# Performance work log

Measured on AMD Instinct MI355X. Metric: run time of the kernel, lower is better.

Reference implementation:

```python
import jax, jax.numpy as jnp
import numpy as np

# ViT-Small config
L, D, H, HD = 12, 384, 6, 64
P, IMG, NCLS = 16, 224, 1000
NPATCH = (IMG // P) ** 2  # 196
GAMMA, MIN_TOKENS, EPS = 0.5, 16, 1e-6
SCALE = HD ** -0.5


def _ln(x, w, b, eps=1e-6):
    mu = jnp.mean(x, axis=-1, keepdims=True)
    var = jnp.var(x, axis=-1, keepdims=True)
    return (x - mu) * jax.lax.rsqrt(var + eps) * w + b


def _qkv_split(xn, w, b):
    # xn: [B, Nt, D] -> q,k,v each [B, H, Nt, HD]
    B, Nt, _ = xn.shape
    qkv = (xn @ w.T + b).reshape(B, Nt, 3, H, HD).transpose(2, 0, 3, 1, 4)
    return qkv[0], qkv[1], qkv[2]


def _vit_forward(x, patch_w, patch_b, cls_token, pos_embed,
                 ln1_w, ln1_b, qkv_w, qkv_b, proj_w, proj_b,
                 ln2_w, ln2_b, fc1_w, fc1_b, fc2_w, fc2_b,
                 norm_w, norm_b, head_w, head_b, keep_schedule=None):
    B = x.shape[0]
    # patch embed: conv stride 16 -> [B, D, 14, 14] -> [B, 196, D]
    xp = jax.lax.conv_general_dilated(x, patch_w, (P, P), 'VALID',
                                      dimension_numbers=('NCHW', 'OIHW', 'NCHW'))
    xp = xp.reshape(B, D, NPATCH).transpose(0, 2, 1) + patch_b
    cls = jnp.broadcast_to(cls_token, (B, 1, D))
    xt = jnp.concatenate([cls, xp], axis=1) + pos_embed  # [B, 197, D]

    N = NPATCH
    prev_mass = jnp.asarray(1.0, jnp.float32)
    schedule = []
    for l in range(L):
        if keep_schedule is not None:
            keep_idx = keep_schedule[l]
        elif N > MIN_TOKENS:
            # CLS-only attention importance scoring (cheap pass)
            xn = _ln(xt, ln1_w[l], ln1_b[l])
            q, k, v = _qkv_split(xn, qkv_w[l], qkv_b[l])
            a_cls = jax.nn.softmax(jnp.einsum('bhqd,bhkd->bhqk', q[:, :, :1], k) * SCALE, axis=-1)[:, :, 0, :]  # [B,H,Nt]
            vnorm = jnp.linalg.norm(v, axis=-1)  # [B,H,Nt]
            imp = (a_cls * vnorm).mean(axis=1)   # [B,Nt]
            imp_p = imp[:, 1:]                   # patch importance
            mass = jnp.mean(imp_p.sum(-1) / (imp.sum(-1) + EPS))
            keep_ratio = float(jnp.clip(GAMMA * mass / (prev_mass + EPS), 0.0, 1.0))
            N_next = max(MIN_TOKENS, int(N * keep_ratio))
            if N_next < N:
                scores = imp_p.mean(0)  # shared keep set across batch (index_select semantics)
                top = jax.lax.top_k(scores, N_next)[1]
                keep_idx = jnp.concatenate([jnp.zeros((1,), jnp.int32),
                                            jnp.sort(top).astype(jnp.int32) + 1])
            else:
                keep_idx = None
            prev_mass = mass
        else:
            keep_idx = None
        schedule.append(keep_idx)
        if keep_idx is not None:
            xt = jnp.take(xt, keep_idx, axis=1)
            N = int(keep_idx.shape[0]) - 1

        # full transformer block on surviving tokens
        Nt = xt.shape[1]
        xn = _ln(xt, ln1_w[l], ln1_b[l])
        q, k, v = _qkv_split(xn, qkv_w[l], qkv_b[l])
        a = jax.nn.softmax(jnp.einsum('bhqd,bhkd->bhqk', q, k) * SCALE, axis=-1)
        o = jnp.einsum('bhqk,bhkd->bhqd', a, v).transpose(0, 2, 1, 3).reshape(B, Nt, D)
        xt = xt + o @ proj_w[l].T + proj_b[l]
        h = _ln(xt, ln2_w[l], ln2_b[l])
        h = jax.nn.gelu(h @ fc1_w[l].T + fc1_b[l], approximate=False)
        xt = xt + h @ fc2_w[l].T + fc2_b[l]

    xt = _ln(xt, norm_w, norm_b)
    logits = xt[:, 0] @ head_w.T + head_b
    return logits, schedule


def setup_inputs() -> dict:
    key = jax.random.key(0)
    ks = jax.random.split(key, 10)
    rn = lambda k, s, sc=0.02: jax.random.normal(k, s, jnp.float32) * sc
    return {
        'x': jax.random.normal(ks[0], (64, 3, IMG, IMG), jnp.float32),
        'patch_w': rn(ks[1], (D, 3, P, P)),
        'patch_b': jnp.zeros((D,), jnp.float32),
        'cls_token': rn(ks[2], (1, 1, D)),
        'pos_embed': rn(ks[3], (1, NPATCH + 1, D)),
        'ln1_w': jnp.ones((L, D), jnp.float32), 'ln1_b': jnp.zeros((L, D), jnp.float32),
        'qkv_w': rn(ks[4], (L, 3 * D, D)), 'qkv_b': jnp.zeros((L, 3 * D), jnp.float32),
        'proj_w': rn(ks[5], (L, D, D)), 'proj_b': jnp.zeros((L, D), jnp.float32),
        'ln2_w': jnp.ones((L, D), jnp.float32), 'ln2_b': jnp.zeros((L, D), jnp.float32),
        'fc1_w': rn(ks[6], (L, 4 * D, D)), 'fc1_b': jnp.zeros((L, 4 * D), jnp.float32),
        'fc2_w': rn(ks[7], (L, D, 4 * D)), 'fc2_b': jnp.zeros((L, D), jnp.float32),
        'norm_w': jnp.ones((D,), jnp.float32), 'norm_b': jnp.zeros((D,), jnp.float32),
        'head_w': rn(ks[8], (NCLS, D)), 'head_b': jnp.zeros((NCLS,), jnp.float32),
    }


def reference(x, patch_w, patch_b, cls_token, pos_embed, ln1_w, ln1_b, qkv_w, qkv_b,
              proj_w, proj_b, ln2_w, ln2_b, fc1_w, fc1_b, fc2_w, fc2_b,
              norm_w, norm_b, head_w, head_b):
    logits, _ = _vit_forward(x, patch_w, patch_b, cls_token, pos_embed, ln1_w, ln1_b,
                             qkv_w, qkv_b, proj_w, proj_b, ln2_w, ln2_b,
                             fc1_w, fc1_b, fc2_w, fc2_b, norm_w, norm_b, head_w, head_b)
    return logits
```

## Files before the change

kernel.cpp:

```cpp
#include <hip/hip_runtime.h>
#include <hip/hip_bf16.h>

static constexpr int kL = 12;
static constexpr int kD = 384;
static constexpr int kH = 6;
static constexpr int kB = 64;
static constexpr int kNP = 196;
static constexpr int kBAND = 197;
static constexpr int kNCLS = 1000;
static constexpr float kSCALE = 0.125f;
static constexpr float kEPS = 1e-6f;
static constexpr size_t kWQ = (size_t)kB * kH * kBAND * 64;

typedef __attribute__((ext_vector_type(8))) short short8;
typedef __attribute__((ext_vector_type(4))) float f32x4;

__device__ __forceinline__ float gelu_f(float x) {
    return 0.5f * x * (1.0f + erff(x * 0.70710678118654752440f));
}
__device__ __forceinline__ unsigned short f2bf(float x) {
    __hip_bfloat16 h = __float2bfloat16(x);
    return *(unsigned short*)&h;
}

__global__ __launch_bounds__(384) void k_init(int* si, float* sf,
                                              const float* __restrict__ cls,
                                              const float* __restrict__ pos,
                                              float* __restrict__ xtA) {
    int b = blockIdx.x, c = threadIdx.x;
    xtA[(size_t)b * kBAND * kD + c] = cls[c] + pos[c];
    if (b == 0 && c == 0) { si[0] = kBAND; sf[0] = 1.0f; }
}

__global__ __launch_bounds__(256) void k_cvtall(
    const float* __restrict__ s0, const float* __restrict__ s1, const float* __restrict__ s2,
    const float* __restrict__ s3, const float* __restrict__ s4,
    __hip_bfloat16* __restrict__ d0, __hip_bfloat16* __restrict__ d1, __hip_bfloat16* __restrict__ d2,
    __hip_bfloat16* __restrict__ d3, __hip_bfloat16* __restrict__ d4) {
    const int c0 = 73728, c1 = 1400832, c2 = 1843200, c3 = 3612672, c4 = 5382144;
    int stride = gridDim.x * 256;
    for (int i = blockIdx.x * 256 + threadIdx.x; i < c4; i += stride) {
        const float* src; __hip_bfloat16* dst; int off;
        if (i < c0)      { src = s0; dst = d0; off = i; }
        else if (i < c1) { src = s1; dst = d1; off = i - c0; }
        else if (i < c2) { src = s2; dst = d2; off = i - c1; }
        else if (i < c3) { src = s3; dst = d3; off = i - c2; }
        else             { src = s4; dst = d4; off = i - c3; }
        float4 v = ((const float4*)src)[off];
        dst[4 * off + 0] = __float2bfloat16(v.x);
        dst[4 * off + 1] = __float2bfloat16(v.y);
        dst[4 * off + 2] = __float2bfloat16(v.z);
        dst[4 * off + 3] = __float2bfloat16(v.w);
    }
}

__global__ __launch_bounds__(256) void k_im2col(const float* __restrict__ x, __hip_bfloat16* __restrict__ A) {
    int pt = blockIdx.x;
    int b = pt / kNP, t = pt - b * kNP;
    int py = t / 14, px = t - py * 14;
    const float* xb = x + (size_t)b * 3 * 224 * 224;
    __hip_bfloat16* arow = A + (size_t)pt * 768;
    for (int k = threadIdx.x; k < 768; k += 256) {
        int c = k >> 8;
        int r = k & 255;
        int ky = r >> 4, kx = r & 15;
        arow[k] = __float2bfloat16(xb[((size_t)c * 224 + py * 16 + ky) * 224 + px * 16 + kx]);
    }
}

template<int OUT_BF16, int ACT_GELU, int MODE, int LNA>
__global__ __launch_bounds__(256) void k_mgemm(
    const void* __restrict__ Av, int lda,
    const unsigned short* __restrict__ W, int K,
    const float* __restrict__ bias,
    void* __restrict__ Cv, int ldc,
    const float* __restrict__ R,
    const int* __restrict__ keepR,
    const float* __restrict__ lnw, const float* __restrict__ lnb,
    int rT, int nT, int band,
    const int* __restrict__ NtPtr, int ntConst)
{
    __shared__ __align__(16) unsigned char pool[18432];
    unsigned short (*As)[72] = (unsigned short (*)[72])pool;
    unsigned short (*Ws)[72] = (unsigned short (*)[72])(pool + 9216);
    float (*Cs)[66] = (float (*)[66])pool;
    unsigned short (*Cu)[76] = (unsigned short (*)[76])pool;
    __shared__ float mus[64], rss[64];

    int Nt = NtPtr ? NtPtr[0] : ntConst;
    unsigned int rowsTotal = (unsigned int)kB * (unsigned int)Nt;

    int L = blockIdx.x;
    int xcd = L & 7;
    int m = L >> 3;
    int n = m % nT;
    int r = (m / nT) * 8 + xcd;
    if (r >= rT) return;
    unsigned int r0 = (unsigned int)r * 64;
    int n0 = n * 64;
    if (r0 >= rowsTotal) return;

    int tid = threadIdx.x;
    int srow = tid >> 3;
    int scol = (tid & 7) << 3;

    unsigned int rv0 = r0 + srow, rv1 = r0 + srow + 32;
    bool v0 = rv0 < rowsTotal, v1 = rv1 < rowsTotal;
    const unsigned short* ah0 = nullptr; const unsigned short* ah1 = nullptr;
    const float* af0 = nullptr; const float* af1 = nullptr;
    if (v0) {
        unsigned int bb = rv0 / (unsigned int)Nt, tt = rv0 - bb * Nt;
        size_t prow = (size_t)bb * band + tt;
        if (LNA) af0 = (const float*)Av + prow * lda;
        else     ah0 = (const unsigned short*)Av + prow * lda;
    }
    if (v1) {
        unsigned int bb = rv1 / (unsigned int)Nt, tt = rv1 - bb * Nt;
        size_t prow = (size_t)bb * band + tt;
        if (LNA) af1 = (const float*)Av + prow * lda;
        else     ah1 = (const unsigned short*)Av + prow * lda;
    }
    const unsigned short* wp0 = W + (size_t)(n0 + srow) * K;
    const unsigned short* wp1 = W + (size_t)(n0 + srow + 32) * K;

    float mu0 = 0.f, rs0 = 0.f, mu1 = 0.f, rs1 = 0.f;
    if (LNA) {
        int sr = tid >> 2, part = tid & 3;
        unsigned int rv = r0 + sr;
        float s1 = 0.f, s2 = 0.f;
        if (rv < rowsTotal) {
            unsigned int bb = rv / (unsigned int)Nt, tt = rv - bb * Nt;
            const float* rp = (const float*)Av + ((size_t)bb * band + tt) * lda + part * 4;
#pragma unroll
            for (int kk = 0; kk < 24; ++kk) {
                float4 q4 = *(const float4*)(rp + kk * 16);
                s1 += q4.x + q4.y + q4.z + q4.w;
                s2 += q4.x * q4.x + q4.y * q4.y + q4.z * q4.z + q4.w * q4.w;
            }
        }
        s1 += __shfl_xor(s1, 1, 64); s2 += __shfl_xor(s2, 1, 64);
        s1 += __shfl_xor(s1, 2, 64); s2 += __shfl_xor(s2, 2, 64);
        if (part == 0) {
            float mu = s1 * (1.f / 384.f);
            float var = fmaxf(s2 * (1.f / 384.f) - mu * mu, 0.f);
            mus[sr] = mu; rss[sr] = rsqrtf(var + kEPS);
        }
        __syncthreads();
        mu0 = mus[srow]; rs0 = rss[srow];
        mu1 = mus[srow + 32]; rs1 = rss[srow + 32];
    }

    int wave = tid >> 6, lane = tid & 63;
    int wr32 = ((wave >> 1) & 1) * 32, wc32 = (wave & 1) * 32;
    int l15 = lane & 15, l4 = lane >> 4;

    f32x4 acc00 = {}, acc01 = {}, acc10 = {}, acc11 = {};

    for (int k0 = 0; k0 < K; k0 += 64) {
        uint4 zero = make_uint4(0, 0, 0, 0);
        uint4 a0 = zero, a1 = zero;
        uint4 w0 = *(const uint4*)(wp0 + k0 + scol);
        uint4 w1 = *(const uint4*)(wp1 + k0 + scol);
        if (LNA) {
            float4 lw0 = *(const float4*)(lnw + k0 + scol);
            float4 lw1 = *(const float4*)(lnw + k0 + scol + 4);
            float4 lb0 = *(const float4*)(lnb + k0 + scol);
            float4 lb1 = *(const float4*)(lnb + k0 + scol + 4);
            if (v0) {
                float4 x0 = *(const float4*)(af0 + k0 + scol);
                float4 x1 = *(const float4*)(af0 + k0 + scol + 4);
                unsigned short p[8];
                p[0] = f2bf((x0.x - mu0) * rs0 * lw0.x + lb0.x);
                p[1] = f2bf((x0.y - mu0) * rs0 * lw0.y + lb0.y);
                p[2] = f2bf((x0.z - mu0) * rs0 * lw0.z + lb0.z);
                p[3] = f2bf((x0.w - mu0) * rs0 * lw0.w + lb0.w);
                p[4] = f2bf((x1.x - mu0) * rs0 * lw1.x + lb1.x);
                p[5] = f2bf((x1.y - mu0) * rs0 * lw1.y + lb1.y);
                p[6] = f2bf((x1.z - mu0) * rs0 * lw1.z + lb1.z);
                p[7] = f2bf((x1.w - mu0) * rs0 * lw1.w + lb1.w);
                a0 = *(uint4*)p;
            }
            if (v1) {
                float4 x0 = *(const float4*)(af1 + k0 + scol);
                float4 x1 = *(const float4*)(af1 + k0 + scol + 4);
                unsigned short p[8];
                p[0] = f2bf((x0.x - mu1) * rs1 * lw0.x + lb0.x);
                p[1] = f2bf((x0.y - mu1) * rs1 * lw0.y + lb0.y);
                p[2] = f2bf((x0.z - mu1) * rs1 * lw0.z + lb0.z);
                p[3] = f2bf((x0.w - mu1) * rs1 * lw0.w + lb0.w);
                p[4] = f2bf((x1.x - mu1) * rs1 * lw1.x + lb1.x);
                p[5] = f2bf((x1.y - mu1) * rs1 * lw1.y + lb1.y);
                p[6] = f2bf((x1.z - mu1) * rs1 * lw1.z + lb1.z);
                p[7] = f2bf((x1.w - mu1) * rs1 * lw1.w + lb1.w);
                a1 = *(uint4*)p;
            }
        } else {
            a0 = v0 ? *(const uint4*)(ah0 + k0 + scol) : zero;
            a1 = v1 ? *(const uint4*)(ah1 + k0 + scol) : zero;
        }
        __syncthreads();
        *(uint4*)&As[srow][scol] = a0;
        *(uint4*)&As[srow + 32][scol] = a1;
        *(uint4*)&Ws[srow][scol] = w0;
        *(uint4*)&Ws[srow + 32][scol] = w1;
        __syncthreads();
#pragma unroll
        for (int ks = 0; ks < 2; ++ks) {
            short8 af_0 = *(const short8*)&As[wr32 + l15][ks * 32 + l4 * 8];
            short8 af_1 = *(const short8*)&As[wr32 + 16 + l15][ks * 32 + l4 * 8];
            short8 bf_0 = *(const short8*)&Ws[wc32 + l15][ks * 32 + l4 * 8];
            short8 bf_1 = *(const short8*)&Ws[wc32 + 16 + l15][ks * 32 + l4 * 8];
            acc00 = __builtin_amdgcn_mfma_f32_16x16x32_bf16(af_0, bf_0, acc00, 0, 0, 0);
            acc01 = __builtin_amdgcn_mfma_f32_16x16x32_bf16(af_0, bf_1, acc01, 0, 0, 0);
            acc10 = __builtin_amdgcn_mfma_f32_16x16x32_bf16(af_1, bf_0, acc10, 0, 0, 0);
            acc11 = __builtin_amdgcn_mfma_f32_16x16x32_bf16(af_1, bf_1, acc11, 0, 0, 0);
        }
    }

    __syncthreads();
    f32x4 accs[2][2] = { { acc00, acc01 }, { acc10, acc11 } };
#pragma unroll
    for (int fi = 0; fi < 2; ++fi) {
        int lrow = wr32 + fi * 16 + l4 * 4;
        unsigned int rvb = r0 + lrow;
#pragma unroll
        for (int fj = 0; fj < 2; ++fj) {
            int lcol = wc32 + fj * 16 + l15;
            float bv = bias ? bias[n0 + lcol] : 0.f;
#pragma unroll
            for (int rr = 0; rr < 4; ++rr) {
                unsigned int rv = rvb + rr;
                float v = accs[fi][fj][rr] + bv;
                if (ACT_GELU) v = gelu_f(v);
                if (MODE == 2) {
                    if (rv < rowsTotal) {
                        unsigned int bb = rv / (unsigned int)Nt;
                        unsigned int tt = rv - bb * (unsigned int)Nt;
                        v += R[(size_t)(tt + 1) * kD + n0 + lcol];
                    }
                } else if (R && rv < rowsTotal) {
                    unsigned int bb = rv / (unsigned int)Nt;
                    unsigned int tt = rv - bb * (unsigned int)Nt;
                    size_t rrow = keepR ? ((size_t)bb * band + keepR[tt]) : ((size_t)bb * band + tt);
                    v += R[rrow * ldc + n0 + lcol];
                }
                if (OUT_BF16) Cu[lrow + rr][lcol] = f2bf(v);
                else          Cs[lrow + rr][lcol] = v;
            }
        }
    }
    __syncthreads();

    if (OUT_BF16) {
#pragma unroll
        for (int i = 0; i < 2; ++i) {
            int id = tid + (i << 8);
            int row = id >> 3, c2 = id & 7;
            unsigned int rv = r0 + row;
            if (rv < rowsTotal) {
                unsigned int bb = rv / (unsigned int)Nt;
                unsigned int tt = rv - bb * (unsigned int)Nt;
                size_t prow = (size_t)bb * band + tt;
                uint4 val = *(const uint4*)&Cu[row][c2 << 3];
                *(uint4*)((__hip_bfloat16*)Cv + prow * ldc + n0 + (c2 << 3)) = val;
            }
        }
    } else {
#pragma unroll
        for (int i = 0; i < 4; ++i) {
            int id = tid + (i << 8);
            int row = id >> 4, c4 = id & 15;
            unsigned int rv = r0 + row;
            if (rv < rowsTotal) {
                unsigned int bb = rv / (unsigned int)Nt;
                unsigned int tt = rv - bb * (unsigned int)Nt;
                float4 val = *(const float4*)&Cs[row][c4 << 2];
                if (MODE == 1) {
                    int which = n0 >= 768 ? 2 : (n0 >= 384 ? 1 : 0);
                    int hh = (n0 - which * 384) >> 6;
                    *(float4*)((float*)Cv + (size_t)which * kWQ +
                               (((size_t)bb * kH + hh) * kBAND + tt) * 64 + (c4 << 2)) = val;
                } else if (MODE == 2) {
                    *(float4*)((float*)Cv + ((size_t)bb * kBAND + tt + 1) * ldc + n0 + (c4 << 2)) = val;
                } else {
                    *(float4*)((float*)Cv + ((size_t)bb * band + tt) * ldc + n0 + (c4 << 2)) = val;
                }
            }
        }
    }
}

__global__ __launch_bounds__(256) void k_decA(const float* __restrict__ qsplit,
                                              float* __restrict__ imph, float* __restrict__ sabh,
                                              const int* __restrict__ si) {
    int Nt = si[0];
    if (Nt - 1 <= 16) return;
    int tid = threadIdx.x;
    int bh = blockIdx.x;
    __shared__ float red[256];
    __shared__ float qs[64];
    const float* qp = qsplit + (size_t)bh * kBAND * 64;
    const float* kp = qsplit + kWQ + (size_t)bh * kBAND * 64;
    const float* vp = qsplit + 2 * kWQ + (size_t)bh * kBAND * 64;
    if (tid < 64) qs[tid] = qp[tid];
    __syncthreads();
    float s = -INFINITY, vn = 0.f;
    if (tid < Nt) {
        const float* krow = kp + ((size_t)tid << 6);
        const float* vrow = vp + ((size_t)tid << 6);
        float a = 0.f, v2 = 0.f;
#pragma unroll
        for (int d = 0; d < 64; d += 4) {
            float4 k4 = *(const float4*)(krow + d);
            float4 v4 = *(const float4*)(vrow + d);
            a += qs[d] * k4.x + qs[d + 1] * k4.y + qs[d + 2] * k4.z + qs[d + 3] * k4.w;
            v2 += v4.x * v4.x + v4.y * v4.y + v4.z * v4.z + v4.w * v4.w;
        }
        s = a * kSCALE;
        vn = sqrtf(v2);
    }
    red[tid] = s; __syncthreads();
    for (int st = 128; st; st >>= 1) { if (tid < st) red[tid] = fmaxf(red[tid], red[tid + st]); __syncthreads(); }
    float mmax = red[0]; __syncthreads();
    float e = (tid < Nt) ? expf(s - mmax) : 0.f;
    red[tid] = e; __syncthreads();
    for (int st = 128; st; st >>= 1) { if (tid < st) red[tid] += red[tid + st]; __syncthreads(); }
    float inv = 1.f / red[0];
    float val = e * inv * vn;
    if (tid < Nt) imph[(size_t)bh * kBAND + tid] = val;
    __syncthreads();
    red[tid] = (tid < Nt) ? val : 0.f; __syncthreads();
    for (int st = 128; st; st >>= 1) { if (tid < st) red[tid] += red[tid + st]; __syncthreads(); }
    if (tid == 0) { sabh[2 * bh] = red[0]; sabh[2 * bh + 1] = val; }
}

__global__ __launch_bounds__(256) void k_decB(int* __restrict__ si, float* __restrict__ sf,
                                              const float* __restrict__ imph,
                                              const float* __restrict__ sabh,
                                              int* __restrict__ keep) {
    int Nt = si[0];
    int tid = threadIdx.x;
    if (Nt - 1 <= 16) {
        for (int j = tid; j < Nt; j += 256) keep[j] = j;
        return;
    }
    int N = Nt - 1;
    __shared__ float red[256];
    float v = 0.f;
    if (tid < kB) {
        float sa = 0.f, i0 = 0.f;
#pragma unroll
        for (int hh = 0; hh < kH; ++hh) {
            sa += sabh[2 * (tid * kH + hh)];
            i0 += sabh[2 * (tid * kH + hh) + 1];
        }
        sa *= (1.f / 6.f); i0 *= (1.f / 6.f);
        v = (sa - i0) / (sa + kEPS);
    }
    red[tid] = v; __syncthreads();
    for (int st = 128; st; st >>= 1) { if (tid < st) red[tid] += red[tid + st]; __syncthreads(); }
    float mass = red[0] * (1.f / 64.f);
    float prev = sf[0];
    float ratio = 0.5f * mass / (prev + kEPS);
    ratio = fminf(fmaxf(ratio, 0.f), 1.f);
    int N_next = (int)((double)N * (double)ratio);
    if (N_next < 16) N_next = 16;
    if (tid == 0) sf[0] = mass;
    __syncthreads();
    if (N_next >= N) {
        for (int j = tid; j < Nt; j += 256) keep[j] = j;
        return;
    }
    __shared__ float sc[200];
    __shared__ int flag[200];
    if (tid < N) {
        float a0 = 0.f, a1 = 0.f, a2 = 0.f, a3 = 0.f;
        const float* p = imph + tid + 1;
#pragma unroll 4
        for (int q = 0; q < kB * kH; q += 4) {
            a0 += p[(size_t)(q + 0) * kBAND];
            a1 += p[(size_t)(q + 1) * kBAND];
            a2 += p[(size_t)(q + 2) * kBAND];
            a3 += p[(size_t)(q + 3) * kBAND];
        }
        sc[tid] = (a0 + a1) + (a2 + a3);
    }
    __syncthreads();
    if (tid < N) {
        float s2 = sc[tid];
        int rank = 0;
        for (int i = 0; i < N; ++i) {
            float o2 = sc[i];
            rank += (o2 > s2) || (o2 == s2 && i < tid);
        }
        flag[tid] = (rank < N_next) ? 1 : 0;
    }
    __syncthreads();
    if (tid == 0) {
        keep[0] = 0;
        int pos = 1;
        for (int j = 0; j < N; ++j) if (flag[j]) keep[pos++] = j + 1;
        si[0] = N_next + 1;
    }
}

__global__ __launch_bounds__(256) void k_attn2(const float* __restrict__ qsplit,
                                               __hip_bfloat16* __restrict__ o,
                                               const int* __restrict__ si,
                                               const int* __restrict__ keep) {
    __shared__ __align__(16) unsigned short Kb[224][72];
    __shared__ __align__(16) unsigned short Vt[64][228];
    __shared__ __align__(16) unsigned short Pb[4][16][228];
    int Nt = si[0];
    int bh = blockIdx.x;
    int b = bh / kH, h = bh - b * kH;
    int tid = threadIdx.x, w = tid >> 6, lane = tid & 63;
    int l15 = lane & 15, l4 = lane >> 4;
    int nJT = (Nt + 15) >> 4;
    int nKT = (Nt + 31) >> 5;
    int NTP = nKT << 5;

    const float* qb = qsplit + (size_t)bh * kBAND * 64;
    const float* kb = qsplit + kWQ + (size_t)bh * kBAND * 64;
    const float* vb = qsplit + 2 * kWQ + (size_t)bh * kBAND * 64;

    {
        int rr = tid >> 3;
        int c8 = (tid & 7) << 3;
        for (int r = rr; r < NTP; r += 32) {
            unsigned short ks[8], vs[8];
#pragma unroll
            for (int e = 0; e < 8; ++e) { ks[e] = 0; vs[e] = 0; }
            if (r < Nt) {
                int old = keep[r];
                const float* kr = kb + ((size_t)old << 6) + c8;
                const float* vr = vb + ((size_t)old << 6) + c8;
                float4 k0 = *(const float4*)kr, k1 = *(const float4*)(kr + 4);
                float4 vv0 = *(const float4*)vr, vv1 = *(const float4*)(vr + 4);
                ks[0] = f2bf(k0.x); ks[1] = f2bf(k0.y); ks[2] = f2bf(k0.z); ks[3] = f2bf(k0.w);
                ks[4] = f2bf(k1.x); ks[5] = f2bf(k1.y); ks[6] = f2bf(k1.z); ks[7] = f2bf(k1.w);
                vs[0] = f2bf(vv0.x); vs[1] = f2bf(vv0.y); vs[2] = f2bf(vv0.z); vs[3] = f2bf(vv0.w);
                vs[4] = f2bf(vv1.x); vs[5] = f2bf(vv1.y); vs[6] = f2bf(vv1.z); vs[7] = f2bf(vv1.w);
            }
            *(uint4*)&Kb[r][c8] = *(uint4*)ks;
#pragma unroll
            for (int e = 0; e < 8; ++e) Vt[c8 + e][r] = vs[e];
        }
    }
    __syncthreads();

    for (int strip = w; strip < nJT; strip += 4) {
        int tq = (strip << 4) + l15;
        int told = (tq < Nt) ? keep[tq] : 0;
        const float* qrow = qb + ((size_t)told << 6) + (l4 << 3);
        float4 q0 = *(const float4*)(qrow),      q1 = *(const float4*)(qrow + 4);
        float4 q2 = *(const float4*)(qrow + 32), q3 = *(const float4*)(qrow + 36);
        unsigned short qa[8], qc[8];
        qa[0] = f2bf(q0.x); qa[1] = f2bf(q0.y); qa[2] = f2bf(q0.z); qa[3] = f2bf(q0.w);
        qa[4] = f2bf(q1.x); qa[5] = f2bf(q1.y); qa[6] = f2bf(q1.z); qa[7] = f2bf(q1.w);
        qc[0] = f2bf(q2.x); qc[1] = f2bf(q2.y); qc[2] = f2bf(q2.z); qc[3] = f2bf(q2.w);
        qc[4] = f2bf(q3.x); qc[5] = f2bf(q3.y); qc[6] = f2bf(q3.z); qc[7] = f2bf(q3.w);
        short8 qf0 = *(short8*)qa;
        short8 qf1 = *(short8*)qc;

        f32x4 sv[13];
#pragma unroll
        for (int jt = 0; jt < 13; ++jt) {
            if (jt < nJT) {
                const unsigned short* kr = &Kb[(jt << 4) + l15][l4 << 3];
                short8 kf0 = *(const short8*)(kr);
                short8 kf1 = *(const short8*)(kr + 32);
                f32x4 a = {};
                a = __builtin_amdgcn_mfma_f32_16x16x32_bf16(qf0, kf0, a, 0, 0, 0);
                a = __builtin_amdgcn_mfma_f32_16x16x32_bf16(qf1, kf1, a, 0, 0, 0);
                sv[jt] = a;
            }
        }
        float mx[4] = { -INFINITY, -INFINITY, -INFINITY, -INFINITY };
#pragma unroll
        for (int jt = 0; jt < 13; ++jt) if (jt < nJT) {
            bool ok = ((jt << 4) + l15) < Nt;
#pragma unroll
            for (int r = 0; r < 4; ++r) {
                float s = ok ? sv[jt][r] * kSCALE : -INFINITY;
                sv[jt][r] = s;
                mx[r] = fmaxf(mx[r], s);
            }
        }
#pragma unroll
        for (int r = 0; r < 4; ++r) {
            mx[r] = fmaxf(mx[r], __shfl_xor(mx[r], 1, 64));
            mx[r] = fmaxf(mx[r], __shfl_xor(mx[r], 2, 64));
            mx[r] = fmaxf(mx[r], __shfl_xor(mx[r], 4, 64));
            mx[r] = fmaxf(mx[r], __shfl_xor(mx[r], 8, 64));
        }
        float sm[4] = { 0.f, 0.f, 0.f, 0.f };
#pragma unroll
        for (int jt = 0; jt < 13; ++jt) if (jt < nJT) {
#pragma unroll
            for (int r = 0; r < 4; ++r) {
                float p = expf(sv[jt][r] - mx[r]);
                sv[jt][r] = p;
                sm[r] += p;
            }
        }
#pragma unroll
        for (int r = 0; r < 4; ++r) {
            sm[r] += __shfl_xor(sm[r], 1, 64);
            sm[r] += __shfl_xor(sm[r], 2, 64);
            sm[r] += __shfl_xor(sm[r], 4, 64);
            sm[r] += __shfl_xor(sm[r], 8, 64);
            sm[r] = 1.f / sm[r];
        }
#pragma unroll
        for (int jt = 0; jt < 13; ++jt) if (jt < nJT) {
#pragma unroll
            for (int r = 0; r < 4; ++r)
                Pb[w][(l4 << 2) + r][(jt << 4) + l15] = f2bf(sv[jt][r] * sm[r]);
        }
        for (int c = (nJT << 4) + lane; c < NTP; c += 64) {
#pragma unroll
            for (int rr2 = 0; rr2 < 16; ++rr2) Pb[w][rr2][c] = 0;
        }
        asm volatile("s_waitcnt lgkmcnt(0)" ::: "memory");
        __builtin_amdgcn_sched_barrier(0);

        f32x4 oacc[4] = { {}, {}, {}, {} };
#pragma unroll
        for (int kt = 0; kt < 7; ++kt) if (kt < nKT) {
            short8 pf = *(const short8*)&Pb[w][l15][(kt << 5) + (l4 << 3)];
#pragma unroll
            for (int dt = 0; dt < 4; ++dt) {
                short8 vf = *(const short8*)&Vt[(dt << 4) + l15][(kt << 5) + (l4 << 3)];
                oacc[dt] = __builtin_amdgcn_mfma_f32_16x16x32_bf16(pf, vf, oacc[dt], 0, 0, 0);
            }
        }
#pragma unroll
        for (int dt = 0; dt < 4; ++dt) {
#pragma unroll
            for (int r = 0; r < 4; ++r) {
                int tqo = (strip << 4) + (l4 << 2) + r;
                if (tqo < Nt)
                    o[((size_t)b * kBAND + tqo) * kD + h * 64 + (dt << 4) + l15] =
                        __float2bfloat16(oacc[dt][r]);
            }
        }
    }
}

__global__ __launch_bounds__(256) void k_head(const float* __restrict__ X,
                                              const float* __restrict__ nw, const float* __restrict__ nb,
                                              const float* __restrict__ hw, const float* __restrict__ hb,
                                              float* __restrict__ out) {
    int b = blockIdx.x >> 2;
    int tid = threadIdx.x;
    __shared__ float xs[384];
    __shared__ float red[256];
    const float* row = X + (size_t)b * kBAND * kD;
    float s1 = 0.f, s2 = 0.f;
    for (int c = tid; c < 384; c += 256) { float v = row[c]; xs[c] = v; s1 += v; s2 += v * v; }
    red[tid] = s1; __syncthreads();
    for (int st = 128; st; st >>= 1) { if (tid < st) red[tid] += red[tid + st]; __syncthreads(); }
    float sum = red[0]; __syncthreads();
    red[tid] = s2; __syncthreads();
    for (int st = 128; st; st >>= 1) { if (tid < st) red[tid] += red[tid + st]; __syncthreads(); }
    float sq = red[0];
    float mu = sum * (1.f / 384.f);
    float var = fmaxf(sq * (1.f / 384.f) - mu * mu, 0.f);
    float rs = rsqrtf(var + kEPS);
    __syncthreads();
    for (int c = tid; c < 384; c += 256) xs[c] = (xs[c] - mu) * rs * nw[c] + nb[c];
    __syncthreads();
    int n = ((blockIdx.x & 3) << 8) + tid;
    if (n >= kNCLS) return;
    const float* wrow = hw + (size_t)n * kD;
    float acc = 0.f;
#pragma unroll 8
    for (int d = 0; d < kD; d += 4) {
        float4 w4 = *(const float4*)(wrow + d);
        acc += xs[d] * w4.x + xs[d + 1] * w4.y + xs[d + 2] * w4.z + xs[d + 3] * w4.w;
    }
    out[(size_t)b * kNCLS + n] = acc + hb[n];
}

extern "C" void kernel_launch(void* const* d_in, const int* in_sizes, int n_in,
                              void* d_out, int out_size, void* d_ws, size_t ws_size,
                              hipStream_t stream) {
    const float* x       = (const float*)d_in[0];
    const float* patch_w = (const float*)d_in[1];
    const float* patch_b = (const float*)d_in[2];
    const float* cls_tok = (const float*)d_in[3];
    const float* pos     = (const float*)d_in[4];
    const float* ln1w    = (const float*)d_in[5];
    const float* ln1b    = (const float*)d_in[6];
    const float* qkvw    = (const float*)d_in[7];
    const float* qkvb    = (const float*)d_in[8];
    const float* projw   = (const float*)d_in[9];
    const float* projb   = (const float*)d_in[10];
    const float* ln2w    = (const float*)d_in[11];
    const float* ln2b    = (const float*)d_in[12];
    const float* fc1w    = (const float*)d_in[13];
    const float* fc1b    = (const float*)d_in[14];
    const float* fc2w    = (const float*)d_in[15];
    const float* fc2b    = (const float*)d_in[16];
    const float* normw   = (const float*)d_in[17];
    const float* normb   = (const float*)d_in[18];
    const float* headw   = (const float*)d_in[19];
    const float* headb   = (const float*)d_in[20];
    float* out = (float*)d_out;

    char* ws = (char*)d_ws;
    const size_t MB = 1024ull * 1024ull;
    int*   si   = (int*)ws;
    float* sf   = (float*)(ws + 64);
    int*   keep = (int*)(ws + 256);
    float* sabh = (float*)(ws + 4096);
    float* imph = (float*)(ws + 16384);
    float* xtA  = (float*)(ws + 1 * MB);
    float* xtB  = (float*)(ws + 21 * MB);
    __hip_bfloat16* obuf = (__hip_bfloat16*)(ws + 41 * MB);
    __hip_bfloat16* Aim    = (__hip_bfloat16*)(ws + 51 * MB);
    float*          qsplit = (float*)(ws + 51 * MB);
    __hip_bfloat16* hbuf   = (__hip_bfloat16*)(ws + 51 * MB);
    __hip_bfloat16* wpat = (__hip_bfloat16*)(ws + 110 * MB);
    __hip_bfloat16* wqkv = (__hip_bfloat16*)(ws + 111 * MB);
    __hip_bfloat16* wprj = (__hip_bfloat16*)(ws + 122 * MB);
    __hip_bfloat16* wfc1 = (__hip_bfloat16*)(ws + 126 * MB);
    __hip_bfloat16* wfc2 = (__hip_bfloat16*)(ws + 141 * MB);

    k_init<<<64, 384, 0, stream>>>(si, sf, cls_tok, pos, xtA);
    k_cvtall<<<2048, 256, 0, stream>>>(patch_w, qkvw, projw, fc1w, fc2w,
                                       wpat, wqkv, wprj, wfc1, wfc2);

    k_im2col<<<kB * kNP, 256, 0, stream>>>(x, Aim);
    k_mgemm<0, 0, 2, 0><<<8 * 6 * 25, 256, 0, stream>>>(
        (const void*)Aim, 768, (const unsigned short*)wpat, 768,
        patch_b, xtA, kD, pos, (const int*)nullptr,
        (const float*)nullptr, (const float*)nullptr,
        196, 6, 196, (const int*)nullptr, 196);

    float* cur = xtA; float* oth = xtB;
    for (int l = 0; l < kL; ++l) {
        const float* l1w = ln1w + l * kD;  const float* l1b = ln1b + l * kD;
        const __hip_bfloat16* qw = wqkv + (size_t)l * 1152 * kD;
        const float* qb = qkvb + l * 1152;
        const __hip_bfloat16* pw = wprj + (size_t)l * kD * kD;
        const float* pb = projb + l * kD;
        const float* l2w = ln2w + l * kD;  const float* l2b = ln2b + l * kD;
        const __hip_bfloat16* f1w = wfc1 + (size_t)l * 1536 * kD;
        const float* f1b = fc1b + l * 1536;
        const __hip_bfloat16* f2w = wfc2 + (size_t)l * kD * 1536;
        const float* f2b = fc2b + l * kD;

        k_mgemm<0, 0, 1, 1><<<8 * 18 * 25, 256, 0, stream>>>(
            (const void*)cur, kD, (const unsigned short*)qw, kD,
            qb, qsplit, 1152, (const float*)nullptr, (const int*)nullptr,
            l1w, l1b, 197, 18, kBAND, si, 0);
        k_decA<<<kB * kH, 256, 0, stream>>>(qsplit, imph, sabh, si);
        k_decB<<<1, 256, 0, stream>>>(si, sf, imph, sabh, keep);
        k_attn2<<<kB * kH, 256, 0, stream>>>(qsplit, obuf, si, keep);
        k_mgemm<0, 0, 0, 0><<<8 * 6 * 25, 256, 0, stream>>>(
            (const void*)obuf, kD, (const unsigned short*)pw, kD,
            pb, oth, kD, cur, keep,
            (const float*)nullptr, (const float*)nullptr,
            197, 6, kBAND, si, 0);
        { float* tmp = cur; cur = oth; oth = tmp; }
        k_mgemm<1, 1, 0, 1><<<8 * 24 * 25, 256, 0, stream>>>(
            (const void*)cur, kD, (const unsigned short*)f1w, kD,
            f1b, hbuf, 1536, (const float*)nullptr, (const int*)nullptr,
            l2w, l2b, 197, 24, kBAND, si, 0);
        k_mgemm<0, 0, 0, 0><<<8 * 6 * 25, 256, 0, stream>>>(
            (const void*)hbuf, 1536, (const unsigned short*)f2w, 1536,
            f2b, cur, kD, cur, (const int*)nullptr,
            (const float*)nullptr, (const float*)nullptr,
            197, 6, kBAND, si, 0);
    }

    k_head<<<kB * 4, 256, 0, stream>>>(cur, normw, normb, headw, headb, out);
}
```

Measured before the change: 1.299 ms.

## Emit per-row LayerNorm partial stats from GEMM epilogues and rework decA dot products

```diff
diff --git a/kernel.cpp b/kernel.cpp
--- a/kernel.cpp
+++ b/kernel.cpp
@@ -26,10 +26,26 @@
 __global__ __launch_bounds__(384) void k_init(int* si, float* sf,
                                               const float* __restrict__ cls,
                                               const float* __restrict__ pos,
-                                              float* __restrict__ xtA) {
+                                              float* __restrict__ xtA,
+                                              float2* __restrict__ pstats) {
     int b = blockIdx.x, c = threadIdx.x;
-    xtA[(size_t)b * kBAND * kD + c] = cls[c] + pos[c];
-    if (b == 0 && c == 0) { si[0] = kBAND; sf[0] = 1.0f; }
+    float v = cls[c] + pos[c];
+    xtA[(size_t)b * kBAND * kD + c] = v;
+    __shared__ float r1[384], r2[384];
+    r1[c] = v; r2[c] = v * v;
+    __syncthreads();
+    if (c < 128) { r1[c] += r1[c + 128] + r1[c + 256]; r2[c] += r2[c + 128] + r2[c + 256]; }
+    __syncthreads();
+    for (int st = 64; st; st >>= 1) {
+        if (c < st) { r1[c] += r1[c + st]; r2[c] += r2[c + st]; }
+        __syncthreads();
+    }
+    if (c == 0) {
+        pstats[(size_t)(b * kBAND) * 8 + 0] = make_float2(r1[0], r2[0]);
+#pragma unroll
+        for (int nn = 1; nn < 6; ++nn) pstats[(size_t)(b * kBAND) * 8 + nn] = make_float2(0.f, 0.f);
+        if (b == 0) { si[0] = kBAND; sf[0] = 1.0f; }
+    }
 }
 
 __global__ __launch_bounds__(256) void k_cvtall(
@@ -68,7 +84,7 @@
     }
 }
 
-template<int OUT_BF16, int ACT_GELU, int MODE, int LNA>
+template<int OUT_BF16, int ACT_GELU, int MODE, int LNA, int STATS>
 __global__ __launch_bounds__(256) void k_mgemm(
     const void* __restrict__ Av, int lda,
     const unsigned short* __restrict__ W, int K,
@@ -78,7 +94,8 @@
     const int* __restrict__ keepR,
     const float* __restrict__ lnw, const float* __restrict__ lnb,
     int rT, int nT, int band,
-    const int* __restrict__ NtPtr, int ntConst)
+    const int* __restrict__ NtPtr, int ntConst,
+    const float2* __restrict__ pstatsIn, float2* __restrict__ pstatsOut)
 {
     __shared__ __align__(16) unsigned char pool[18432];
     unsigned short (*As)[72] = (unsigned short (*)[72])pool;
@@ -125,25 +142,20 @@
 
     float mu0 = 0.f, rs0 = 0.f, mu1 = 0.f, rs1 = 0.f;
     if (LNA) {
-        int sr = tid >> 2, part = tid & 3;
-        unsigned int rv = r0 + sr;
-        float s1 = 0.f, s2 = 0.f;
-        if (rv < rowsTotal) {
-            unsigned int bb = rv / (unsigned int)Nt, tt = rv - bb * Nt;
-            const float* rp = (const float*)Av + ((size_t)bb * band + tt) * lda + part * 4;
-#pragma unroll
-            for (int kk = 0; kk < 24; ++kk) {
-                float4 q4 = *(const float4*)(rp + kk * 16);
-                s1 += q4.x + q4.y + q4.z + q4.w;
-                s2 += q4.x * q4.x + q4.y * q4.y + q4.z * q4.z + q4.w * q4.w;
-            }
-        }
-        s1 += __shfl_xor(s1, 1, 64); s2 += __shfl_xor(s2, 1, 64);
-        s1 += __shfl_xor(s1, 2, 64); s2 += __shfl_xor(s2, 2, 64);
-        if (part == 0) {
-            float mu = s1 * (1.f / 384.f);
-            float var = fmaxf(s2 * (1.f / 384.f) - mu * mu, 0.f);
-            mus[sr] = mu; rss[sr] = rsqrtf(var + kEPS);
+        if (tid < 64) {
+            unsigned int rv = r0 + tid;
+            float mu = 0.f, rsd = 0.f;
+            if (rv < rowsTotal) {
+                unsigned int bb = rv / (unsigned int)Nt, tt = rv - bb * Nt;
+                const float2* ps = pstatsIn + ((size_t)bb * band + tt) * 8;
+                float s1 = 0.f, s2 = 0.f;
+#pragma unroll
+                for (int nn = 0; nn < 6; ++nn) { float2 p = ps[nn]; s1 += p.x; s2 += p.y; }
+                mu = s1 * (1.f / 384.f);
+                float var = fmaxf(s2 * (1.f / 384.f) - mu * mu, 0.f);
+                rsd = rsqrtf(var + kEPS);
+            }
+            mus[tid] = mu; rss[tid] = rsd;
         }
         __syncthreads();
         mu0 = mus[srow]; rs0 = rss[srow];
@@ -285,6 +297,20 @@
                 } else {
                     *(float4*)((float*)Cv + ((size_t)bb * band + tt) * ldc + n0 + (c4 << 2)) = val;
                 }
+                if (STATS) {
+                    float s1 = (val.x + val.y) + (val.z + val.w);
+                    float s2 = (val.x * val.x + val.y * val.y) + (val.z * val.z + val.w * val.w);
+#pragma unroll
+                    for (int off = 1; off < 16; off <<= 1) {
+                        s1 += __shfl_xor(s1, off, 64);
+                        s2 += __shfl_xor(s2, off, 64);
+                    }
+                    if (c4 == 0) {
+                        size_t sridx = (MODE == 2) ? ((size_t)bb * kBAND + tt + 1)
+                                                   : ((size_t)bb * band + tt);
+                        pstatsOut[sridx * 8 + n] = make_float2(s1, s2);
+                    }
+                }
             }
         }
     }
@@ -295,30 +321,38 @@
                                               const int* __restrict__ si) {
     int Nt = si[0];
     if (Nt - 1 <= 16) return;
-    int tid = threadIdx.x;
+    int tid = threadIdx.x, w = tid >> 6, lane = tid & 63;
     int bh = blockIdx.x;
+    __shared__ float qs[64];
+    __shared__ float sdot[224], svn[224];
     __shared__ float red[256];
-    __shared__ float qs[64];
     const float* qp = qsplit + (size_t)bh * kBAND * 64;
     const float* kp = qsplit + kWQ + (size_t)bh * kBAND * 64;
     const float* vp = qsplit + 2 * kWQ + (size_t)bh * kBAND * 64;
     if (tid < 64) qs[tid] = qp[tid];
     __syncthreads();
-    float s = -INFINITY, vn = 0.f;
-    if (tid < Nt) {
-        const float* krow = kp + ((size_t)tid << 6);
-        const float* vrow = vp + ((size_t)tid << 6);
-        float a = 0.f, v2 = 0.f;
-#pragma unroll
-        for (int d = 0; d < 64; d += 4) {
-            float4 k4 = *(const float4*)(krow + d);
-            float4 v4 = *(const float4*)(vrow + d);
-            a += qs[d] * k4.x + qs[d + 1] * k4.y + qs[d + 2] * k4.z + qs[d + 3] * k4.w;
-            v2 += v4.x * v4.x + v4.y * v4.y + v4.z * v4.z + v4.w * v4.w;
-        }
-        s = a * kSCALE;
-        vn = sqrtf(v2);
-    }
+    float qv = qs[lane];
+    for (int j = w; j < Nt; j += 8) {
+        int j2 = j + 4;
+        bool has2 = j2 < Nt;
+        float k1 = kp[(size_t)j * 64 + lane];
+        float v1 = vp[(size_t)j * 64 + lane];
+        float k2 = has2 ? kp[(size_t)j2 * 64 + lane] : 0.f;
+        float v2 = has2 ? vp[(size_t)j2 * 64 + lane] : 0.f;
+        float p1 = qv * k1, n1 = v1 * v1;
+        float p2 = qv * k2, n2 = v2 * v2;
+#pragma unroll
+        for (int off = 1; off < 64; off <<= 1) {
+            p1 += __shfl_xor(p1, off, 64); n1 += __shfl_xor(n1, off, 64);
+            p2 += __shfl_xor(p2, off, 64); n2 += __shfl_xor(n2, off, 64);
+        }
+        if (lane == 0) {
+            sdot[j] = p1 * kSCALE; svn[j] = sqrtf(n1);
+            if (has2) { sdot[j2] = p2 * kSCALE; svn[j2] = sqrtf(n2); }
+        }
+    }
+    __syncthreads();
+    float s = (tid < Nt) ? sdot[tid] : -INFINITY;
     red[tid] = s; __syncthreads();
     for (int st = 128; st; st >>= 1) { if (tid < st) red[tid] = fmaxf(red[tid], red[tid + st]); __syncthreads(); }
     float mmax = red[0]; __syncthreads();
@@ -326,10 +360,10 @@
     red[tid] = e; __syncthreads();
     for (int st = 128; st; st >>= 1) { if (tid < st) red[tid] += red[tid + st]; __syncthreads(); }
     float inv = 1.f / red[0];
-    float val = e * inv * vn;
+    float val = (tid < Nt) ? e * inv * svn[tid] : 0.f;
     if (tid < Nt) imph[(size_t)bh * kBAND + tid] = val;
     __syncthreads();
-    red[tid] = (tid < Nt) ? val : 0.f; __syncthreads();
+    red[tid] = val; __syncthreads();
     for (int st = 128; st; st >>= 1) { if (tid < st) red[tid] += red[tid + st]; __syncthreads(); }
     if (tid == 0) { sabh[2 * bh] = red[0]; sabh[2 * bh + 1] = val; }
 }
@@ -627,17 +661,19 @@
     __hip_bfloat16* wprj = (__hip_bfloat16*)(ws + 122 * MB);
     __hip_bfloat16* wfc1 = (__hip_bfloat16*)(ws + 126 * MB);
     __hip_bfloat16* wfc2 = (__hip_bfloat16*)(ws + 141 * MB);
-
-    k_init<<<64, 384, 0, stream>>>(si, sf, cls_tok, pos, xtA);
+    float2* pstats = (float2*)(ws + 156 * MB);
+
+    k_init<<<64, 384, 0, stream>>>(si, sf, cls_tok, pos, xtA, pstats);
     k_cvtall<<<2048, 256, 0, stream>>>(patch_w, qkvw, projw, fc1w, fc2w,
                                        wpat, wqkv, wprj, wfc1, wfc2);
 
     k_im2col<<<kB * kNP, 256, 0, stream>>>(x, Aim);
-    k_mgemm<0, 0, 2, 0><<<8 * 6 * 25, 256, 0, stream>>>(
+    k_mgemm<0, 0, 2, 0, 1><<<8 * 6 * 25, 256, 0, stream>>>(
         (const void*)Aim, 768, (const unsigned short*)wpat, 768,
         patch_b, xtA, kD, pos, (const int*)nullptr,
         (const float*)nullptr, (const float*)nullptr,
-        196, 6, 196, (const int*)nullptr, 196);
+        196, 6, 196, (const int*)nullptr, 196,
+        (const float2*)nullptr, pstats);
 
     float* cur = xtA; float* oth = xtB;
     for (int l = 0; l < kL; ++l) {
@@ -652,28 +688,32 @@
         const __hip_bfloat16* f2w = wfc2 + (size_t)l * kD * 1536;
         const float* f2b = fc2b + l * kD;
 
-        k_mgemm<0, 0, 1, 1><<<8 * 18 * 25, 256, 0, stream>>>(
+        k_mgemm<0, 0, 1, 1, 0><<<8 * 18 * 25, 256, 0, stream>>>(
             (const void*)cur, kD, (const unsigned short*)qw, kD,
             qb, qsplit, 1152, (const float*)nullptr, (const int*)nullptr,
-            l1w, l1b, 197, 18, kBAND, si, 0);
+            l1w, l1b, 197, 18, kBAND, si, 0,
+            (const float2*)pstats, (float2*)nullptr);
         k_decA<<<kB * kH, 256, 0, stream>>>(qsplit, imph, sabh, si);
         k_decB<<<1, 256, 0, stream>>>(si, sf, imph, sabh, keep);
         k_attn2<<<kB * kH, 256, 0, stream>>>(qsplit, obuf, si, keep);
-        k_mgemm<0, 0, 0, 0><<<8 * 6 * 25, 256, 0, stream>>>(
+        k_mgemm<0, 0, 0, 0, 1><<<8 * 6 * 25, 256, 0, stream>>>(
             (const void*)obuf, kD, (const unsigned short*)pw, kD,
             pb, oth, kD, cur, keep,
             (const float*)nullptr, (const float*)nullptr,
-            197, 6, kBAND, si, 0);
+            197, 6, kBAND, si, 0,
+            (const float2*)nullptr, pstats);
         { float* tmp = cur; cur = oth; oth = tmp; }
-        k_mgemm<1, 1, 0, 1><<<8 * 24 * 25, 256, 0, stream>>>(
+        k_mgemm<1, 1, 0, 1, 0><<<8 * 24 * 25, 256, 0, stream>>>(
             (const void*)cur, kD, (const unsigned short*)f1w, kD,
             f1b, hbuf, 1536, (const float*)nullptr, (const int*)nullptr,
-            l2w, l2b, 197, 24, kBAND, si, 0);
-        k_mgemm<0, 0, 0, 0><<<8 * 6 * 25, 256, 0, stream>>>(
+            l2w, l2b, 197, 24, kBAND, si, 0,
+            (const float2*)pstats, (float2*)nullptr);
+        k_mgemm<0, 0, 0, 0, 1><<<8 * 6 * 25, 256, 0, stream>>>(
             (const void*)hbuf, 1536, (const unsigned short*)f2w, 1536,
             f2b, cur, kD, cur, (const int*)nullptr,
             (const float*)nullptr, (const float*)nullptr,
-            197, 6, kBAND, si, 0);
+            197, 6, kBAND, si, 0,
+            (const float2*)nullptr, pstats);
     }
 
     k_head<<<kB * 4, 256, 0, stream>>>(cur, normw, normb, headw, headb, out);
```

New measurement: 1.262 ms. -2.8%, faster.
